# Kernel tuning notes

Measured on AMD Instinct MI355X. Metric: run time of the kernel, lower is better.

The kernel has to match this reference:

```python
import jax, jax.numpy as jnp
import numpy as np

H = 256   # hidden_size
F = 1024  # feedforward_size


def setup_inputs() -> dict:
    key = jax.random.key(0)
    ks = jax.random.split(key, 12)
    s = 1.0 / np.sqrt(H)
    sf = 1.0 / np.sqrt(F)
    return {
        "x": jax.random.normal(ks[0], (4, 4096, H), dtype=jnp.float32),
        "wq": jax.random.uniform(ks[1], (H, H), jnp.float32, -s, s),
        "bq": jax.random.uniform(ks[2], (H,), jnp.float32, -s, s),
        "wk": jax.random.uniform(ks[3], (H, H), jnp.float32, -s, s),
        "bk": jax.random.uniform(ks[4], (H,), jnp.float32, -s, s),
        "wv": jax.random.uniform(ks[5], (H, H), jnp.float32, -s, s),
        "bv": jax.random.uniform(ks[6], (H,), jnp.float32, -s, s),
        "w1": jax.random.uniform(ks[7], (H, F), jnp.float32, -s, s),
        "b1": jax.random.uniform(ks[8], (F,), jnp.float32, -s, s),
        "w2": jax.random.uniform(ks[9], (F, H), jnp.float32, -sf, sf),
        "b2": jax.random.uniform(ks[10], (H,), jnp.float32, -sf, sf),
        "ln_g": jnp.ones((H,), jnp.float32),
        "ln_b": jnp.zeros((H,), jnp.float32),
    }


def _layernorm(x, g, b, eps=1e-5):
    mu = jnp.mean(x, axis=-1, keepdims=True)
    var = jnp.var(x, axis=-1, keepdims=True)
    return (x - mu) * jax.lax.rsqrt(var + eps) * g + b


def reference(x, wq, bq, wk, bk, wv, bv, w1, b1, w2, b2, ln_g, ln_b):
    # Self-attention (single head, head_dim = hidden)
    q = x @ wq + bq            # [b, s, H]
    k = x @ wk + bk
    v = x @ wv + bv
    scores = jnp.einsum("bsh,bth->bst", q, k) / np.sqrt(H).astype(np.float32)
    a = jax.nn.softmax(scores, axis=-1)      # [b, s, s] (materialized, as in source)
    attn = jnp.einsum("bst,bth->bsh", a, v)  # [b, s, H]
    # FeedForward: lnrm(attn + lin2(relu(lin1(attn))))  (dropout = identity, eval)
    h = jax.nn.relu(attn @ w1 + b1)
    y = attn + h @ w2 + b2
    return _layernorm(y, ln_g, ln_b)
```

## Files before the change

### kernel.cpp

```cpp
#include <hip/hip_runtime.h>
#include <hip/hip_bf16.h>

typedef __bf16 bf16;
typedef __attribute__((ext_vector_type(8))) __bf16 bf16x8;
typedef __attribute__((ext_vector_type(4))) __bf16 bf16x4;
typedef __attribute__((ext_vector_type(4))) float f32x4;

#define MFMA_16x16x32(a, b, c) __builtin_amdgcn_mfma_f32_16x16x32_bf16(a, b, c, 0, 0, 0)

#define BATCH 4
#define SEQ   4096
#define HID   256
#define FFD   1024
#define MTOT  (BATCH * SEQ)
#define NSPLIT 2

__global__ __launch_bounds__(256) void prep_kernel(
    const float* __restrict__ x,
    const float* __restrict__ wq, const float* __restrict__ wk, const float* __restrict__ wv,
    const float* __restrict__ w1, const float* __restrict__ w2,
    bf16* __restrict__ xb,
    bf16* __restrict__ wqT, bf16* __restrict__ wkT, bf16* __restrict__ wvT,
    bf16* __restrict__ w1T, bf16* __restrict__ w2T)
{
    int i = blockIdx.x * 256 + threadIdx.x;
    if (i < 1048576) {
        float4 v = ((const float4*)x)[i];
        bf16x4 o;
        o[0] = (bf16)v.x; o[1] = (bf16)v.y; o[2] = (bf16)v.z; o[3] = (bf16)v.w;
        ((bf16x4*)xb)[i] = o;
        return;
    }
    i -= 1048576;
    if (i < 3 * 65536) {
        const float* src = (i < 65536) ? wq : (i < 131072) ? wk : wv;
        bf16* dst = (i < 65536) ? wqT : (i < 131072) ? wkT : wvT;
        int j = i & 65535;
        int r = j >> 8, c = j & 255;
        dst[c * 256 + r] = (bf16)src[j];
        return;
    }
    i -= 3 * 65536;
    if (i < 262144) {
        int r = i >> 10, c = i & 1023;
        w1T[c * 256 + r] = (bf16)w1[i];
        return;
    }
    i -= 262144;
    int r = i >> 8, c = i & 255;
    w2T[c * 1024 + r] = (bf16)w2[i];
}

__global__ __launch_bounds__(256) void qkv_kernel(
    const bf16* __restrict__ xb,
    const bf16* __restrict__ wqT, const bf16* __restrict__ wkT, const bf16* __restrict__ wvT,
    const float* __restrict__ bq, const float* __restrict__ bk, const float* __restrict__ bv,
    bf16* __restrict__ q, bf16* __restrict__ k, bf16* __restrict__ vT)
{
    __shared__ bf16 vt[64][72];
    const int lane = threadIdx.x & 63, wave = threadIdx.x >> 6;
    const int g = lane >> 4, c = lane & 15;
    const int mat = blockIdx.y >> 2;
    const int n0 = (blockIdx.y & 3) * 64;
    const int mblk = blockIdx.x * 64;
    const int m0 = mblk + wave * 16;
    const bf16* wT = (mat == 0) ? wqT : (mat == 1) ? wkT : wvT;
    const float* bias = (mat == 0) ? bq : (mat == 1) ? bk : bv;

    f32x4 acc[4] = {};
    #pragma unroll
    for (int ks = 0; ks < 8; ++ks) {
        bf16x8 a = *(const bf16x8*)(xb + (size_t)(m0 + c) * 256 + ks * 32 + 8 * g);
        #pragma unroll
        for (int nf = 0; nf < 4; ++nf) {
            bf16x8 b = *(const bf16x8*)(wT + (size_t)(n0 + nf * 16 + c) * 256 + ks * 32 + 8 * g);
            acc[nf] = MFMA_16x16x32(a, b, acc[nf]);
        }
    }
    if (mat < 2) {
        bf16* out = (mat == 0) ? q : k;
        #pragma unroll
        for (int nf = 0; nf < 4; ++nf) {
            int n = n0 + nf * 16 + c;
            float bs = bias[n];
            #pragma unroll
            for (int r = 0; r < 4; ++r)
                out[(size_t)(m0 + 4 * g + r) * 256 + n] = (bf16)(acc[nf][r] + bs);
        }
    } else {
        #pragma unroll
        for (int nf = 0; nf < 4; ++nf) {
            int n = n0 + nf * 16 + c;
            float bs = bias[n];
            #pragma unroll
            for (int r = 0; r < 4; ++r)
                vt[nf * 16 + c][wave * 16 + 4 * g + r] = (bf16)(acc[nf][r] + bs);
        }
        __syncthreads();
        int bt = mblk >> 12;
        int s0 = mblk & (SEQ - 1);
        int nl = threadIdx.x >> 2;
        int sc = (threadIdx.x & 3) * 16;
        bf16* dst = vT + ((size_t)bt * 256 + n0 + nl) * SEQ + s0 + sc;
        const bf16x8* sp = (const bf16x8*)&vt[nl][sc];
        ((bf16x8*)dst)[0] = sp[0];
        ((bf16x8*)dst)[1] = sp[1];
    }
}


#define STAGE_GLOAD(KV) do {                                                              \
    _Pragma("unroll")                                                                     \
    for (int i_ = 0; i_ < 4; ++i_) {                                                      \
        int ch_ = i_ * 256 + tid;                                                         \
        kreg[i_] = *(const bf16x8*)(kbase + (size_t)((KV) + (ch_ >> 5)) * 256 + (ch_ & 31) * 8); \
        vreg[i_] = *(const bf16x8*)(vbase + (size_t)(ch_ >> 2) * SEQ + (KV) + (ch_ & 3) * 8);    \
    } } while (0)

#define STAGE_DSWRITE() do {                                                              \
    _Pragma("unroll")                                                                     \
    for (int i_ = 0; i_ < 4; ++i_) {                                                      \
        int ch_ = i_ * 256 + tid;                                                         \
        int kr_ = ch_ >> 5, kcb_ = ch_ & 31;                                              \
        int kf_ = (kcb_ >> 2) * 2 + (kr_ >> 4);                                           \
        int kl_ = (kcb_ & 3) * 16 + (kr_ & 15);                                           \
        *(bf16x8*)&kstage[kf_][kl_ ^ ((kl_ >> 3) & 6)][0] = kreg[i_];                     \
        int vd_ = ch_ >> 2, vs_ = ch_ & 3;                                                \
        int g1_ = 2 * (vs_ & 1), jh_ = (vs_ >> 1) * 4;                                    \
        bf16x4 lo_ = ((const bf16x4*)&vreg[i_])[0];                                       \
        bf16x4 hi_ = ((const bf16x4*)&vreg[i_])[1];                                       \
        *(bf16x4*)&vstage[vd_ >> 4][g1_ * 16 + (vd_ & 15)][jh_]        = lo_;             \
        *(bf16x4*)&vstage[vd_ >> 4][g1_ * 16 + 16 + (vd_ & 15)][jh_]   = hi_;             \
    } } while (0)

#define ATTN_BODY() do {                                                                  \
    f32x4 s0 = {}, s1 = {};                                                               \
    __builtin_amdgcn_s_setprio(1);                                                        \
    _Pragma("unroll")                                                                     \
    for (int ks_ = 0; ks_ < 8; ++ks_) {                                                   \
        bf16x8 k0_ = *(const bf16x8*)&kstage[ks_ * 2 + 0][kln][0];                        \
        bf16x8 k1_ = *(const bf16x8*)&kstage[ks_ * 2 + 1][kln][0];                        \
        s0 = MFMA_16x16x32(k0_, qf[ks_], s0);                                             \
        s1 = MFMA_16x16x32(k1_, qf[ks_], s1);                                             \
    }                                                                                     \
    __builtin_amdgcn_s_setprio(0);                                                        \
    float p_[8];                                                                          \
    _Pragma("unroll")                                                                     \
    for (int r_ = 0; r_ < 4; ++r_) { p_[r_] = s0[r_] * 0.0625f; p_[4 + r_] = s1[r_] * 0.0625f; } \
    float mx = fmaxf(fmaxf(fmaxf(p_[0], p_[1]), fmaxf(p_[2], p_[3])),                     \
                     fmaxf(fmaxf(p_[4], p_[5]), fmaxf(p_[6], p_[7])));                    \
    mx = fmaxf(mx, __shfl_xor(mx, 16));                                                   \
    mx = fmaxf(mx, __shfl_xor(mx, 32));                                                   \
    if (__any(mx > m_run)) {                \
        float mn = fmaxf(m_run, mx);                                                      \
        float a_ = __expf(m_run - mn);                                                    \
        m_run = mn; l_run *= a_;                                                          \
        float a0_ = __shfl(a_, 4 * g + 0), a1_ = __shfl(a_, 4 * g + 1);                   \
        float a2_ = __shfl(a_, 4 * g + 2), a3_ = __shfl(a_, 4 * g + 3);                   \
        _Pragma("unroll")                                                                 \
        for (int nf_ = 0; nf_ < 16; ++nf_) {                                              \
            o[nf_][0] *= a0_; o[nf_][1] *= a1_; o[nf_][2] *= a2_; o[nf_][3] *= a3_;       \
        }                                                                                 \
    }                                                                                     \
    float ls = 0.f;                                                                       \
    _Pragma("unroll")                                                                     \
    for (int j_ = 0; j_ < 8; ++j_) { p_[j_] = __expf(p_[j_] - m_run); ls += p_[j_]; }     \
    ls += __shfl_xor(ls, 16);                                                             \
    ls += __shfl_xor(ls, 32);                                                             \
    l_run += ls;                                                                          \
    bf16x8 pa;                                                                            \
    _Pragma("unroll")                                                                     \
    for (int j_ = 0; j_ < 8; ++j_) pa[j_] = (bf16)p_[j_];                                 \
    __builtin_amdgcn_s_setprio(1);                                                        \
    _Pragma("unroll")                                                                     \
    for (int nf_ = 0; nf_ < 16; ++nf_) {                                                  \
        bf16x8 v_ = *(const bf16x8*)&vstage[nf_][lane][0];                                \
        o[nf_] = MFMA_16x16x32(pa, v_, o[nf_]);                                           \
    }                                                                                     \
    __builtin_amdgcn_s_setprio(0);                                                        \
} while (0)

__global__ __launch_bounds__(256) void attn_kernel(
    const bf16* __restrict__ qb, const bf16* __restrict__ kb, const bf16* __restrict__ vT,
    float* __restrict__ o_part, float* __restrict__ ml_part)
{
    __shared__ bf16 kstage[16][64][8];
    __shared__ bf16 vstage[16][64][8];
    const int tid = threadIdx.x;
    const int lane = tid & 63, wave = tid >> 6;
    const int g = lane >> 4, c = lane & 15;
    const int kln = lane ^ ((lane >> 3) & 6);
    const int xcd = blockIdx.x & 7, qg = blockIdx.x >> 3;
    const int bt = xcd >> 1, split = xcd & 1;
    const int mrow = bt * SEQ + qg * 64 + wave * 16;
    const int kvS = split << 11;

    bf16x8 qf[8];
    #pragma unroll
    for (int ks = 0; ks < 8; ++ks)
        qf[ks] = *(const bf16x8*)(qb + (size_t)(mrow + c) * 256 + ks * 32 + 8 * g);

    f32x4 o[16] = {};
    float m_run = -1e30f, l_run = 0.f;

    const bf16* kbase = kb + (size_t)bt * SEQ * 256;
    const bf16* vbase = vT + (size_t)bt * 256 * SEQ;

    bf16x8 kreg[4], vreg[4];
    STAGE_GLOAD(kvS);
    STAGE_DSWRITE();
    __syncthreads();

    #pragma unroll 1
    for (int t = 0; t < 64; ++t) {
        if (t < 63) STAGE_GLOAD(kvS + (t + 1) * 32);
        ATTN_BODY();
        __syncthreads();
        if (t < 63) {
            STAGE_DSWRITE();
            __syncthreads();
        }
    }

    float linv = 1.f / l_run;
    float l0 = __shfl(linv, 4 * g + 0), l1 = __shfl(linv, 4 * g + 1);
    float l2 = __shfl(linv, 4 * g + 2), l3 = __shfl(linv, 4 * g + 3);
    float* op = o_part + ((size_t)split * MTOT + mrow) * 256;
    #pragma unroll
    for (int nf = 0; nf < 16; ++nf) {
        op[(size_t)(4 * g + 0) * 256 + nf * 16 + c] = o[nf][0] * l0;
        op[(size_t)(4 * g + 1) * 256 + nf * 16 + c] = o[nf][1] * l1;
        op[(size_t)(4 * g + 2) * 256 + nf * 16 + c] = o[nf][2] * l2;
        op[(size_t)(4 * g + 3) * 256 + nf * 16 + c] = o[nf][3] * l3;
    }
    if (g == 0) {
        float2 ml = make_float2(m_run, l_run);
        *(float2*)&ml_part[((size_t)split * MTOT + mrow + c) * 2] = ml;
    }
}

__global__ __launch_bounds__(256) void attn_combine_kernel(
    const float* __restrict__ o_part, const float* __restrict__ ml_part,
    bf16* __restrict__ attn_bf)
{
    const int row = blockIdx.x * 16 + (threadIdx.x >> 4);
    const int c0 = (threadIdx.x & 15) * 16;
    float m[NSPLIT], l[NSPLIT];
    #pragma unroll
    for (int s = 0; s < NSPLIT; ++s) {
        float2 ml = *(const float2*)&ml_part[((size_t)s * MTOT + row) * 2];
        m[s] = ml.x; l[s] = ml.y;
    }
    float M = fmaxf(m[0], m[1]);
    float w[NSPLIT], L = 0.f;
    #pragma unroll
    for (int s = 0; s < NSPLIT; ++s) { w[s] = __expf(m[s] - M) * l[s]; L += w[s]; }
    float Linv = 1.f / L;
    #pragma unroll
    for (int s = 0; s < NSPLIT; ++s) w[s] *= Linv;

    float acc[16] = {};
    #pragma unroll
    for (int s = 0; s < NSPLIT; ++s) {
        const float* op = o_part + ((size_t)s * MTOT + row) * 256 + c0;
        #pragma unroll
        for (int j4 = 0; j4 < 4; ++j4) {
            float4 v = ((const float4*)op)[j4];
            acc[j4 * 4 + 0] += w[s] * v.x; acc[j4 * 4 + 1] += w[s] * v.y;
            acc[j4 * 4 + 2] += w[s] * v.z; acc[j4 * 4 + 3] += w[s] * v.w;
        }
    }
    bf16* dst = attn_bf + (size_t)row * 256 + c0;
    #pragma unroll
    for (int j = 0; j < 16; ++j) dst[j] = (bf16)acc[j];
}

__global__ __launch_bounds__(256) void ffn1_kernel(
    const bf16* __restrict__ attn, const bf16* __restrict__ w1T, const float* __restrict__ b1,
    bf16* __restrict__ h, int m_base)
{
    const int lane = threadIdx.x & 63, wave = threadIdx.x >> 6;
    const int g = lane >> 4, c = lane & 15;
    const int m0 = m_base + blockIdx.x * 64 + wave * 16;
    const int n0 = blockIdx.y * 64;

    f32x4 acc[4] = {};
    #pragma unroll
    for (int ks = 0; ks < 8; ++ks) {
        bf16x8 a = *(const bf16x8*)(attn + (size_t)(m0 + c) * 256 + ks * 32 + 8 * g);
        #pragma unroll
        for (int nf = 0; nf < 4; ++nf) {
            bf16x8 b = *(const bf16x8*)(w1T + (size_t)(n0 + nf * 16 + c) * 256 + ks * 32 + 8 * g);
            acc[nf] = MFMA_16x16x32(a, b, acc[nf]);
        }
    }
    #pragma unroll
    for (int nf = 0; nf < 4; ++nf) {
        int n = n0 + nf * 16 + c;
        float bs = b1[n];
        #pragma unroll
        for (int r = 0; r < 4; ++r) {
            float v = fmaxf(acc[nf][r] + bs, 0.f);
            h[(size_t)(m0 - m_base + 4 * g + r) * FFD + n] = (bf16)v;
        }
    }
}

__global__ __launch_bounds__(64) void ffn2_ln_kernel(
    const bf16* __restrict__ h, const bf16* __restrict__ w2T, const float* __restrict__ b2,
    const bf16* __restrict__ attn_bf, const float* __restrict__ ln_g, const float* __restrict__ ln_b,
    float* __restrict__ out, int m_base)
{
    const int lane = threadIdx.x & 63;
    const int g = lane >> 4, c = lane & 15;
    const int m0 = m_base + blockIdx.x * 16;
    const int mloc = m0 - m_base;

    f32x4 acc[16] = {};
    for (int ks = 0; ks < 32; ++ks) {
        bf16x8 a = *(const bf16x8*)(h + (size_t)(mloc + c) * FFD + ks * 32 + 8 * g);
        #pragma unroll
        for (int nf = 0; nf < 16; ++nf) {
            bf16x8 b = *(const bf16x8*)(w2T + (size_t)(nf * 16 + c) * FFD + ks * 32 + 8 * g);
            acc[nf] = MFMA_16x16x32(a, b, acc[nf]);
        }
    }
    #pragma unroll
    for (int nf = 0; nf < 16; ++nf) {
        int col = nf * 16 + c;
        float bs = b2[col];
        #pragma unroll
        for (int r = 0; r < 4; ++r)
            acc[nf][r] += bs + (float)attn_bf[(size_t)(m0 + 4 * g + r) * 256 + col];
    }
    float sum[4] = {}, sq[4] = {};
    #pragma unroll
    for (int nf = 0; nf < 16; ++nf)
        #pragma unroll
        for (int r = 0; r < 4; ++r) { sum[r] += acc[nf][r]; sq[r] += acc[nf][r] * acc[nf][r]; }
    float mean[4], rstd[4];
    #pragma unroll
    for (int r = 0; r < 4; ++r) {
        float s_ = sum[r], q_ = sq[r];
        s_ += __shfl_xor(s_, 1); s_ += __shfl_xor(s_, 2); s_ += __shfl_xor(s_, 4); s_ += __shfl_xor(s_, 8);
        q_ += __shfl_xor(q_, 1); q_ += __shfl_xor(q_, 2); q_ += __shfl_xor(q_, 4); q_ += __shfl_xor(q_, 8);
        mean[r] = s_ * (1.f / 256.f);
        float var = q_ * (1.f / 256.f) - mean[r] * mean[r];
        rstd[r] = rsqrtf(var + 1e-5f);
    }
    #pragma unroll
    for (int nf = 0; nf < 16; ++nf) {
        int col = nf * 16 + c;
        float gg = ln_g[col], bb = ln_b[col];
        #pragma unroll
        for (int r = 0; r < 4; ++r)
            out[(size_t)(m0 + 4 * g + r) * 256 + col] = (acc[nf][r] - mean[r]) * rstd[r] * gg + bb;
    }
}

extern "C" void kernel_launch(void* const* d_in, const int* in_sizes, int n_in,
                              void* d_out, int out_size, void* d_ws, size_t ws_size,
                              hipStream_t stream) {
    const float* x    = (const float*)d_in[0];
    const float* wq   = (const float*)d_in[1];
    const float* bq   = (const float*)d_in[2];
    const float* wk   = (const float*)d_in[3];
    const float* bk   = (const float*)d_in[4];
    const float* wv   = (const float*)d_in[5];
    const float* bv   = (const float*)d_in[6];
    const float* w1   = (const float*)d_in[7];
    const float* b1   = (const float*)d_in[8];
    const float* w2   = (const float*)d_in[9];
    const float* b2   = (const float*)d_in[10];
    const float* ln_g = (const float*)d_in[11];
    const float* ln_b = (const float*)d_in[12];
    float* out = (float*)d_out;

    char* ws = (char*)d_ws;
    bf16* wqT = (bf16*)(ws + 0);
    bf16* wkT = (bf16*)(ws + 131072);
    bf16* wvT = (bf16*)(ws + 262144);
    bf16* w1T = (bf16*)(ws + 393216);
    bf16* w2T = (bf16*)(ws + 917504);
    bf16* xb  = (bf16*)(ws + 2097152);
    bf16* qb  = (bf16*)(ws + 10485760);
    bf16* kb  = (bf16*)(ws + 18874368);
    bf16* vT  = (bf16*)(ws + 27262976);
    float* o_part  = (float*)(ws + 35651584);
    float* ml_part = (float*)(ws + 69206016);
    bf16* attn_bf = xb;
    bf16* hbuf    = qb;

    const int PREP_N = (1048576 + 3 * 65536 + 2 * 262144) / 256;
    prep_kernel<<<PREP_N, 256, 0, stream>>>(x, wq, wk, wv, w1, w2, xb, wqT, wkT, wvT, w1T, w2T);

    qkv_kernel<<<dim3(MTOT / 64, 12), 256, 0, stream>>>(xb, wqT, wkT, wvT, bq, bk, bv, qb, kb, vT);
    attn_kernel<<<(MTOT / 64) * NSPLIT, 256, 0, stream>>>(qb, kb, vT, o_part, ml_part);
    attn_combine_kernel<<<MTOT / 16, 256, 0, stream>>>(o_part, ml_part, attn_bf);

    const int HALF = MTOT / 2;
    for (int p = 0; p < 2; ++p) {
        ffn1_kernel<<<dim3(HALF / 64, FFD / 64), 256, 0, stream>>>(attn_bf, w1T, b1, hbuf, p * HALF);
        ffn2_ln_kernel<<<HALF / 16, 64, 0, stream>>>(hbuf, w2T, b2, attn_bf, ln_g, ln_b, out, p * HALF);
    }
}
```

Measured before the change: 360.3 us.

## Fuse FFN1 and FFN2+LayerNorm into one kernel with hidden activations in LDS

Replaces the two-pass ffn1/ffn2_ln launches with a single kernel per 16-row tile. Each of four waves computes a 256-column slice of the ReLU hidden layer into a swizzled LDS buffer, then each wave computes a 64-column slice of the second GEMM. LayerNorm statistics are reduced across waves through LDS. This removes the global round-trip of the hidden activations and several launches, at the cost of 32KB of LDS per block and redundant weight reads per 16-row tile.

```diff
diff --git a/kernel.cpp b/kernel.cpp
--- a/kernel.cpp
+++ b/kernel.cpp
@@ -275,86 +275,99 @@
     for (int j = 0; j < 16; ++j) dst[j] = (bf16)acc[j];
 }
 
-__global__ __launch_bounds__(256) void ffn1_kernel(
+__global__ __launch_bounds__(256) void ffn_fused_kernel(
     const bf16* __restrict__ attn, const bf16* __restrict__ w1T, const float* __restrict__ b1,
-    bf16* __restrict__ h, int m_base)
+    const bf16* __restrict__ w2T, const float* __restrict__ b2,
+    const float* __restrict__ ln_g, const float* __restrict__ ln_b,
+    float* __restrict__ out)
 {
+    __shared__ bf16 h_lds[16][1024];
     const int lane = threadIdx.x & 63, wave = threadIdx.x >> 6;
     const int g = lane >> 4, c = lane & 15;
-    const int m0 = m_base + blockIdx.x * 64 + wave * 16;
-    const int n0 = blockIdx.y * 64;
-
-    f32x4 acc[4] = {};
-    #pragma unroll
-    for (int ks = 0; ks < 8; ++ks) {
-        bf16x8 a = *(const bf16x8*)(attn + (size_t)(m0 + c) * 256 + ks * 32 + 8 * g);
+    const int m0 = blockIdx.x * 16;
+
+    const int n1 = wave * 256;
+    {
+        f32x4 acc[16] = {};
+        #pragma unroll
+        for (int ks = 0; ks < 8; ++ks) {
+            bf16x8 a = *(const bf16x8*)(attn + (size_t)(m0 + c) * 256 + ks * 32 + 8 * g);
+            #pragma unroll
+            for (int nf = 0; nf < 16; ++nf) {
+                bf16x8 b = *(const bf16x8*)(w1T + (size_t)(n1 + nf * 16 + c) * 256 + ks * 32 + 8 * g);
+                acc[nf] = MFMA_16x16x32(a, b, acc[nf]);
+            }
+        }
+        #pragma unroll
+        for (int nf = 0; nf < 16; ++nf) {
+            int n = n1 + nf * 16 + c;
+            float bs = b1[n];
+            int chunk = (n >> 3);
+            int off = n & 7;
+            #pragma unroll
+            for (int r = 0; r < 4; ++r) {
+                int row = 4 * g + r;
+                h_lds[row][((chunk ^ (row & 7)) << 3) | off] = (bf16)fmaxf(acc[nf][r] + bs, 0.f);
+            }
+        }
+    }
+    __syncthreads();
+
+    const int n2 = wave * 64;
+    f32x4 acc2[4] = {};
+    #pragma unroll 8
+    for (int ks = 0; ks < 32; ++ks) {
+        int chunk = 4 * ks + g;
+        bf16x8 a = *(const bf16x8*)&h_lds[c][(chunk ^ (c & 7)) << 3];
         #pragma unroll
         for (int nf = 0; nf < 4; ++nf) {
-            bf16x8 b = *(const bf16x8*)(w1T + (size_t)(n0 + nf * 16 + c) * 256 + ks * 32 + 8 * g);
-            acc[nf] = MFMA_16x16x32(a, b, acc[nf]);
-        }
-    }
+            bf16x8 b = *(const bf16x8*)(w2T + (size_t)(n2 + nf * 16 + c) * 1024 + ks * 32 + 8 * g);
+            acc2[nf] = MFMA_16x16x32(a, b, acc2[nf]);
+        }
+    }
+    float sum[4] = {}, sq[4] = {};
     #pragma unroll
     for (int nf = 0; nf < 4; ++nf) {
-        int n = n0 + nf * 16 + c;
-        float bs = b1[n];
+        int col = n2 + nf * 16 + c;
+        float bs = b2[col];
         #pragma unroll
         for (int r = 0; r < 4; ++r) {
-            float v = fmaxf(acc[nf][r] + bs, 0.f);
-            h[(size_t)(m0 - m_base + 4 * g + r) * FFD + n] = (bf16)v;
-        }
-    }
-}
-
-__global__ __launch_bounds__(64) void ffn2_ln_kernel(
-    const bf16* __restrict__ h, const bf16* __restrict__ w2T, const float* __restrict__ b2,
-    const bf16* __restrict__ attn_bf, const float* __restrict__ ln_g, const float* __restrict__ ln_b,
-    float* __restrict__ out, int m_base)
-{
-    const int lane = threadIdx.x & 63;
-    const int g = lane >> 4, c = lane & 15;
-    const int m0 = m_base + blockIdx.x * 16;
-    const int mloc = m0 - m_base;
-
-    f32x4 acc[16] = {};
-    for (int ks = 0; ks < 32; ++ks) {
-        bf16x8 a = *(const bf16x8*)(h + (size_t)(mloc + c) * FFD + ks * 32 + 8 * g);
-        #pragma unroll
-        for (int nf = 0; nf < 16; ++nf) {
-            bf16x8 b = *(const bf16x8*)(w2T + (size_t)(nf * 16 + c) * FFD + ks * 32 + 8 * g);
-            acc[nf] = MFMA_16x16x32(a, b, acc[nf]);
-        }
-    }
-    #pragma unroll
-    for (int nf = 0; nf < 16; ++nf) {
-        int col = nf * 16 + c;
-        float bs = b2[col];
-        #pragma unroll
-        for (int r = 0; r < 4; ++r)
-            acc[nf][r] += bs + (float)attn_bf[(size_t)(m0 + 4 * g + r) * 256 + col];
-    }
-    float sum[4] = {}, sq[4] = {};
-    #pragma unroll
-    for (int nf = 0; nf < 16; ++nf)
-        #pragma unroll
-        for (int r = 0; r < 4; ++r) { sum[r] += acc[nf][r]; sq[r] += acc[nf][r] * acc[nf][r]; }
-    float mean[4], rstd[4];
+            float v = acc2[nf][r] + bs + (float)attn[(size_t)(m0 + 4 * g + r) * 256 + col];
+            acc2[nf][r] = v;
+            sum[r] += v; sq[r] += v * v;
+        }
+    }
     #pragma unroll
     for (int r = 0; r < 4; ++r) {
-        float s_ = sum[r], q_ = sq[r];
-        s_ += __shfl_xor(s_, 1); s_ += __shfl_xor(s_, 2); s_ += __shfl_xor(s_, 4); s_ += __shfl_xor(s_, 8);
-        q_ += __shfl_xor(q_, 1); q_ += __shfl_xor(q_, 2); q_ += __shfl_xor(q_, 4); q_ += __shfl_xor(q_, 8);
-        mean[r] = s_ * (1.f / 256.f);
-        float var = q_ * (1.f / 256.f) - mean[r] * mean[r];
-        rstd[r] = rsqrtf(var + 1e-5f);
-    }
-    #pragma unroll
-    for (int nf = 0; nf < 16; ++nf) {
-        int col = nf * 16 + c;
-        float gg = ln_g[col], bb = ln_b[col];
-        #pragma unroll
-        for (int r = 0; r < 4; ++r)
-            out[(size_t)(m0 + 4 * g + r) * 256 + col] = (acc[nf][r] - mean[r]) * rstd[r] * gg + bb;
+        sum[r] += __shfl_xor(sum[r], 1); sum[r] += __shfl_xor(sum[r], 2);
+        sum[r] += __shfl_xor(sum[r], 4); sum[r] += __shfl_xor(sum[r], 8);
+        sq[r]  += __shfl_xor(sq[r], 1);  sq[r]  += __shfl_xor(sq[r], 2);
+        sq[r]  += __shfl_xor(sq[r], 4);  sq[r]  += __shfl_xor(sq[r], 8);
+    }
+    float* sums = (float*)&h_lds[0][0];
+    __syncthreads();
+    if (c == 0) {
+        #pragma unroll
+        for (int r = 0; r < 4; ++r) {
+            sums[wave * 32 + (4 * g + r) * 2 + 0] = sum[r];
+            sums[wave * 32 + (4 * g + r) * 2 + 1] = sq[r];
+        }
+    }
+    __syncthreads();
+    #pragma unroll
+    for (int r = 0; r < 4; ++r) {
+        int row = 4 * g + r;
+        float S = sums[0 * 32 + row * 2] + sums[1 * 32 + row * 2]
+                + sums[2 * 32 + row * 2] + sums[3 * 32 + row * 2];
+        float Q = sums[0 * 32 + row * 2 + 1] + sums[1 * 32 + row * 2 + 1]
+                + sums[2 * 32 + row * 2 + 1] + sums[3 * 32 + row * 2 + 1];
+        float mean = S * (1.f / 256.f);
+        float rstd = rsqrtf(Q * (1.f / 256.f) - mean * mean + 1e-5f);
+        #pragma unroll
+        for (int nf = 0; nf < 4; ++nf) {
+            int col = n2 + nf * 16 + c;
+            out[(size_t)(m0 + row) * 256 + col] = (acc2[nf][r] - mean) * rstd * ln_g[col] + ln_b[col];
+        }
     }
 }
 
@@ -389,7 +402,6 @@
     float* o_part  = (float*)(ws + 35651584);
     float* ml_part = (float*)(ws + 69206016);
     bf16* attn_bf = xb;
-    bf16* hbuf    = qb;
 
     const int PREP_N = (1048576 + 3 * 65536 + 2 * 262144) / 256;
     prep_kernel<<<PREP_N, 256, 0, stream>>>(x, wq, wk, wv, w1, w2, xb, wqT, wkT, wvT, w1T, w2T);
@@ -397,10 +409,5 @@
     qkv_kernel<<<dim3(MTOT / 64, 12), 256, 0, stream>>>(xb, wqT, wkT, wvT, bq, bk, bv, qb, kb, vT);
     attn_kernel<<<(MTOT / 64) * NSPLIT, 256, 0, stream>>>(qb, kb, vT, o_part, ml_part);
     attn_combine_kernel<<<MTOT / 16, 256, 0, stream>>>(o_part, ml_part, attn_bf);
-
-    const int HALF = MTOT / 2;
-    for (int p = 0; p < 2; ++p) {
-        ffn1_kernel<<<dim3(HALF / 64, FFD / 64), 256, 0, stream>>>(attn_bf, w1T, b1, hbuf, p * HALF);
-        ffn2_ln_kernel<<<HALF / 16, 64, 0, stream>>>(hbuf, w2T, b2, attn_bf, ln_g, ln_b, out, p * HALF);
-    }
-}
+    ffn_fused_kernel<<<MTOT / 16, 256, 0, stream>>>(attn_bf, w1T, b1, w2T, b2, ln_g, ln_b, out);
+}
```

New measurement: 355.3 us. Within noise of the previous version (-1.4%).

## Fuse FFN1 and FFN2+LayerNorm into one kernel keeping hidden activations in registers

Applied to the files above, without the earlier changes.

Replaces the two-pass ffn1 / ffn2_ln launches with a single kernel. Each 64-thread block owns 16 rows and walks the 1024-wide hidden dimension in chunks of 256. For each chunk it computes W1·attn transposed with MFMA, applies bias and ReLU, and repacks the result into bf16 A-operands that feed the W2 MFMA directly. This removes the global write and re-read of the h buffer and cuts launches from four to one. The cost is heavy register pressure (two 16-entry accumulator arrays plus operands). Weights are also re-read per block from cache with split 4-element loads, and the block is small.

```diff
diff --git a/kernel.cpp b/kernel.cpp
--- a/kernel.cpp
+++ b/kernel.cpp
@@ -275,69 +275,73 @@
     for (int j = 0; j < 16; ++j) dst[j] = (bf16)acc[j];
 }
 
-__global__ __launch_bounds__(256) void ffn1_kernel(
+__global__ __launch_bounds__(64) void ffn_fused_kernel(
     const bf16* __restrict__ attn, const bf16* __restrict__ w1T, const float* __restrict__ b1,
-    bf16* __restrict__ h, int m_base)
+    const bf16* __restrict__ w2T, const float* __restrict__ b2,
+    const float* __restrict__ ln_g, const float* __restrict__ ln_b,
+    float* __restrict__ out)
 {
-    const int lane = threadIdx.x & 63, wave = threadIdx.x >> 6;
+    const int lane = threadIdx.x;
     const int g = lane >> 4, c = lane & 15;
-    const int m0 = m_base + blockIdx.x * 64 + wave * 16;
-    const int n0 = blockIdx.y * 64;
-
-    f32x4 acc[4] = {};
-    #pragma unroll
-    for (int ks = 0; ks < 8; ++ks) {
-        bf16x8 a = *(const bf16x8*)(attn + (size_t)(m0 + c) * 256 + ks * 32 + 8 * g);
-        #pragma unroll
-        for (int nf = 0; nf < 4; ++nf) {
-            bf16x8 b = *(const bf16x8*)(w1T + (size_t)(n0 + nf * 16 + c) * 256 + ks * 32 + 8 * g);
-            acc[nf] = MFMA_16x16x32(a, b, acc[nf]);
-        }
-    }
-    #pragma unroll
-    for (int nf = 0; nf < 4; ++nf) {
-        int n = n0 + nf * 16 + c;
-        float bs = b1[n];
-        #pragma unroll
-        for (int r = 0; r < 4; ++r) {
-            float v = fmaxf(acc[nf][r] + bs, 0.f);
-            h[(size_t)(m0 - m_base + 4 * g + r) * FFD + n] = (bf16)v;
-        }
-    }
-}
-
-__global__ __launch_bounds__(64) void ffn2_ln_kernel(
-    const bf16* __restrict__ h, const bf16* __restrict__ w2T, const float* __restrict__ b2,
-    const bf16* __restrict__ attn_bf, const float* __restrict__ ln_g, const float* __restrict__ ln_b,
-    float* __restrict__ out, int m_base)
-{
-    const int lane = threadIdx.x & 63;
-    const int g = lane >> 4, c = lane & 15;
-    const int m0 = m_base + blockIdx.x * 16;
-    const int mloc = m0 - m_base;
-
-    f32x4 acc[16] = {};
-    for (int ks = 0; ks < 32; ++ks) {
-        bf16x8 a = *(const bf16x8*)(h + (size_t)(mloc + c) * FFD + ks * 32 + 8 * g);
-        #pragma unroll
-        for (int nf = 0; nf < 16; ++nf) {
-            bf16x8 b = *(const bf16x8*)(w2T + (size_t)(nf * 16 + c) * FFD + ks * 32 + 8 * g);
-            acc[nf] = MFMA_16x16x32(a, b, acc[nf]);
-        }
-    }
+    const int m0 = blockIdx.x * 16;
+
+    bf16x8 qa[8];
+    #pragma unroll
+    for (int ks = 0; ks < 8; ++ks)
+        qa[ks] = *(const bf16x8*)(attn + (size_t)(m0 + c) * 256 + ks * 32 + 8 * g);
+
+    f32x4 acc2[16] = {};
+    #pragma unroll 1
+    for (int chunk = 0; chunk < 4; ++chunk) {
+        const int nbase = chunk * 256;
+        f32x4 acc1[16] = {};
+        #pragma unroll
+        for (int ks = 0; ks < 8; ++ks) {
+            #pragma unroll
+            for (int nf = 0; nf < 16; ++nf) {
+                bf16x8 w = *(const bf16x8*)(w1T + (size_t)(nbase + nf * 16 + c) * 256 + ks * 32 + 8 * g);
+                acc1[nf] = MFMA_16x16x32(w, qa[ks], acc1[nf]);
+            }
+        }
+        bf16x8 pa[8];
+        #pragma unroll
+        for (int t = 0; t < 8; ++t) {
+            float4 blo = *(const float4*)&b1[nbase + t * 32 + 4 * g];
+            float4 bhi = *(const float4*)&b1[nbase + t * 32 + 16 + 4 * g];
+            pa[t][0] = (bf16)fmaxf(acc1[2 * t][0] + blo.x, 0.f);
+            pa[t][1] = (bf16)fmaxf(acc1[2 * t][1] + blo.y, 0.f);
+            pa[t][2] = (bf16)fmaxf(acc1[2 * t][2] + blo.z, 0.f);
+            pa[t][3] = (bf16)fmaxf(acc1[2 * t][3] + blo.w, 0.f);
+            pa[t][4] = (bf16)fmaxf(acc1[2 * t + 1][0] + bhi.x, 0.f);
+            pa[t][5] = (bf16)fmaxf(acc1[2 * t + 1][1] + bhi.y, 0.f);
+            pa[t][6] = (bf16)fmaxf(acc1[2 * t + 1][2] + bhi.z, 0.f);
+            pa[t][7] = (bf16)fmaxf(acc1[2 * t + 1][3] + bhi.w, 0.f);
+        }
+        #pragma unroll
+        for (int t = 0; t < 8; ++t) {
+            #pragma unroll
+            for (int nf = 0; nf < 16; ++nf) {
+                const bf16* wp = w2T + (size_t)(nf * 16 + c) * 1024 + nbase + t * 32 + 4 * g;
+                bf16x8 w;
+                ((bf16x4*)&w)[0] = *(const bf16x4*)wp;
+                ((bf16x4*)&w)[1] = *(const bf16x4*)(wp + 16);
+                acc2[nf] = MFMA_16x16x32(pa[t], w, acc2[nf]);
+            }
+        }
+    }
+
+    float sum[4] = {}, sq[4] = {};
     #pragma unroll
     for (int nf = 0; nf < 16; ++nf) {
         int col = nf * 16 + c;
         float bs = b2[col];
         #pragma unroll
-        for (int r = 0; r < 4; ++r)
-            acc[nf][r] += bs + (float)attn_bf[(size_t)(m0 + 4 * g + r) * 256 + col];
-    }
-    float sum[4] = {}, sq[4] = {};
-    #pragma unroll
-    for (int nf = 0; nf < 16; ++nf)
-        #pragma unroll
-        for (int r = 0; r < 4; ++r) { sum[r] += acc[nf][r]; sq[r] += acc[nf][r] * acc[nf][r]; }
+        for (int r = 0; r < 4; ++r) {
+            float v = acc2[nf][r] + bs + (float)attn[(size_t)(m0 + 4 * g + r) * 256 + col];
+            acc2[nf][r] = v;
+            sum[r] += v; sq[r] += v * v;
+        }
+    }
     float mean[4], rstd[4];
     #pragma unroll
     for (int r = 0; r < 4; ++r) {
@@ -345,8 +349,7 @@
         s_ += __shfl_xor(s_, 1); s_ += __shfl_xor(s_, 2); s_ += __shfl_xor(s_, 4); s_ += __shfl_xor(s_, 8);
         q_ += __shfl_xor(q_, 1); q_ += __shfl_xor(q_, 2); q_ += __shfl_xor(q_, 4); q_ += __shfl_xor(q_, 8);
         mean[r] = s_ * (1.f / 256.f);
-        float var = q_ * (1.f / 256.f) - mean[r] * mean[r];
-        rstd[r] = rsqrtf(var + 1e-5f);
+        rstd[r] = rsqrtf(q_ * (1.f / 256.f) - mean[r] * mean[r] + 1e-5f);
     }
     #pragma unroll
     for (int nf = 0; nf < 16; ++nf) {
@@ -354,7 +357,7 @@
         float gg = ln_g[col], bb = ln_b[col];
         #pragma unroll
         for (int r = 0; r < 4; ++r)
-            out[(size_t)(m0 + 4 * g + r) * 256 + col] = (acc[nf][r] - mean[r]) * rstd[r] * gg + bb;
+            out[(size_t)(m0 + 4 * g + r) * 256 + col] = (acc2[nf][r] - mean[r]) * rstd[r] * gg + bb;
     }
 }
 
@@ -389,7 +392,6 @@
     float* o_part  = (float*)(ws + 35651584);
     float* ml_part = (float*)(ws + 69206016);
     bf16* attn_bf = xb;
-    bf16* hbuf    = qb;
 
     const int PREP_N = (1048576 + 3 * 65536 + 2 * 262144) / 256;
     prep_kernel<<<PREP_N, 256, 0, stream>>>(x, wq, wk, wv, w1, w2, xb, wqT, wkT, wvT, w1T, w2T);
@@ -397,10 +399,5 @@
     qkv_kernel<<<dim3(MTOT / 64, 12), 256, 0, stream>>>(xb, wqT, wkT, wvT, bq, bk, bv, qb, kb, vT);
     attn_kernel<<<(MTOT / 64) * NSPLIT, 256, 0, stream>>>(qb, kb, vT, o_part, ml_part);
     attn_combine_kernel<<<MTOT / 16, 256, 0, stream>>>(o_part, ml_part, attn_bf);
-
-    const int HALF = MTOT / 2;
-    for (int p = 0; p < 2; ++p) {
-        ffn1_kernel<<<dim3(HALF / 64, FFD / 64), 256, 0, stream>>>(attn_bf, w1T, b1, hbuf, p * HALF);
-        ffn2_ln_kernel<<<HALF / 16, 64, 0, stream>>>(hbuf, w2T, b2, attn_bf, ln_g, ln_b, out, p * HALF);
-    }
-}
+    ffn_fused_kernel<<<MTOT / 16, 64, 0, stream>>>(attn_bf, w1T, b1, w2T, b2, ln_g, ln_b, out);
+}
```

Measured after the change: 456.8 us. 1.27x slower.
